# Kernel tuning notes

Measured on AMD Instinct MI355X. Metric: run time of the kernel, lower is better.

Reference implementation:

```python
import jax, jax.numpy as jnp
import numpy as np

N = 50000   # nodes per channel
E = 800000  # edges per channel
F = 128     # node feature dim
H = 4       # heads
C = 32      # per-head channels (output_dim // heads = 128 // 4)
D = H * C   # output_dim = 128
B = 64      # graphs in batch


def gatv2_conv(x, edge_index, Wl, bl, Wr, br, att, bias):
    """PyG GATv2Conv (share_weights=False, add_self_loops=True, neg_slope=0.2),
    eval mode (attention dropout disabled)."""
    n = x.shape[0]
    loops = jnp.arange(n, dtype=edge_index.dtype)
    src = jnp.concatenate([edge_index[0], loops])  # [E+N]
    dst = jnp.concatenate([edge_index[1], loops])
    xl = (x @ Wl + bl).reshape(n, H, C)  # source transform
    xr = (x @ Wr + br).reshape(n, H, C)  # target transform
    s = xl[src] + xr[dst]                              # [E+N, H, C]
    e = jnp.einsum('ehc,hc->eh', jax.nn.leaky_relu(s, 0.2), att)  # [E+N, H]
    emax = jax.ops.segment_max(e, dst, num_segments=n)            # softmax over incoming edges
    ee = jnp.exp(e - emax[dst])
    denom = jax.ops.segment_sum(ee, dst, num_segments=n)
    alpha = ee / jnp.maximum(denom[dst], 1e-16)                   # [E+N, H]
    out = jax.ops.segment_sum(alpha[:, :, None] * xl[src], dst, num_segments=n)  # [N, H, C]
    return out.reshape(n, D) + bias


def gep(x, batch, num_graphs):
    """global_mean_pool"""
    s = jax.ops.segment_sum(x, batch, num_segments=num_graphs)
    cnt = jax.ops.segment_sum(jnp.ones((x.shape[0],), x.dtype), batch, num_segments=num_graphs)
    return s / jnp.maximum(cnt, 1.0)[:, None]


def lrelu(x):  # nn.LeakyReLU() default slope 0.01
    return jax.nn.leaky_relu(x, 0.01)


def _branch_params(key, scale=0.05):
    ks = jax.random.split(key, 8)
    return dict(
        Wl=jax.random.normal(ks[0], (F, D), jnp.float32) * scale,
        bl=jnp.zeros((D,), jnp.float32),
        Wr=jax.random.normal(ks[1], (F, D), jnp.float32) * scale,
        br=jnp.zeros((D,), jnp.float32),
        att=jax.random.normal(ks[2], (H, C), jnp.float32) * scale,
        bias=jnp.zeros((D,), jnp.float32),
        fcW=jax.random.normal(ks[3], (D, D), jnp.float32) * scale,
        fcb=jnp.zeros((D,), jnp.float32),
    )


def setup_inputs() -> dict:
    key = jax.random.key(0)
    k = jax.random.split(key, 12)
    inp = {
        'ch1_x': jax.random.normal(k[0], (N, F), jnp.float32),
        'ch1_edge_index': jax.random.randint(k[1], (2, E), 0, N, jnp.int32),
        'ch1_batch': jnp.sort(jax.random.randint(k[2], (N,), 0, B, jnp.int32)),
        'ch2_x': jax.random.normal(k[3], (N, F), jnp.float32),
        'ch2_edge_index': jax.random.randint(k[4], (2, E), 0, N, jnp.int32),
        'ch2_batch': jnp.sort(jax.random.randint(k[5], (N,), 0, B, jnp.int32)),
    }
    p1 = _branch_params(k[6]); p2 = _branch_params(k[7])
    for name, v in p1.items():
        inp['p1_' + name] = v
    for name, v in p2.items():
        inp['p2_' + name] = v
    inp['fc1_W'] = jax.random.normal(k[8], (2 * D, D), jnp.float32) * 0.05
    inp['fc1_b'] = jnp.zeros((D,), jnp.float32)
    inp['fc2_W'] = jax.random.normal(k[9], (D, 16), jnp.float32) * 0.05
    inp['fc2_b'] = jnp.zeros((16,), jnp.float32)
    inp['out_W'] = jax.random.normal(k[10], (16, 1), jnp.float32) * 0.05
    inp['out_b'] = jnp.zeros((1,), jnp.float32)
    return inp


def reference(ch1_x, ch1_edge_index, ch1_batch, ch2_x, ch2_edge_index, ch2_batch,
              p1_Wl, p1_bl, p1_Wr, p1_br, p1_att, p1_bias, p1_fcW, p1_fcb,
              p2_Wl, p2_bl, p2_Wr, p2_br, p2_att, p2_bias, p2_fcW, p2_fcb,
              fc1_W, fc1_b, fc2_W, fc2_b, out_W, out_b):
    # branch 1 (dropout = identity in eval mode)
    x = gatv2_conv(ch1_x, ch1_edge_index, p1_Wl, p1_bl, p1_Wr, p1_br, p1_att, p1_bias)
    x = lrelu(x)
    x = gep(x, ch1_batch, B)
    x = lrelu(x @ p1_fcW + p1_fcb)
    # branch 2
    xt = gatv2_conv(ch2_x, ch2_edge_index, p2_Wl, p2_bl, p2_Wr, p2_br, p2_att, p2_bias)
    xt = lrelu(xt)
    xt = gep(xt, ch2_batch, B)
    xt = lrelu(xt @ p2_fcW + p2_fcb)
    # head
    xc = jnp.concatenate([x, xt], axis=1)          # [B, 2D]
    xc = lrelu(xc @ fc1_W + fc1_b)
    xc = lrelu(xc @ fc2_W + fc2_b)
    return xc @ out_W + out_b                      # [B, 1]
```

## Files before the change

### kernel.cpp

```cpp
#include <hip/hip_runtime.h>
#include <hip/hip_bf16.h>
#include <math.h>

#define F_DIM 128
#define B_GRAPHS 64
#define AGG_WAVES 8

__device__ __forceinline__ float lrelu(float v, float s) {
    return v > 0.f ? v : s * v;
}

__device__ __forceinline__ int lower_bound_i(const int* __restrict__ a, int n, int v) {
    int lo = 0, hi = n;
    while (lo < hi) {
        int mid = (lo + hi) >> 1;
        if (a[mid] < v) lo = mid + 1; else hi = mid;
    }
    return lo;
}

__global__ void count2_k(const int* __restrict__ ei0, const int* __restrict__ ei1,
                         int* __restrict__ c0, int* __restrict__ c1, int E) {
    const int* ei = blockIdx.y ? ei1 : ei0;
    int* cnt = blockIdx.y ? c1 : c0;
    int i = blockIdx.x * blockDim.x + threadIdx.x;
    if (i < E) atomicAdd(cnt + ei[E + i], 1);
}

__global__ __launch_bounds__(1024) void scan2_k(const int* __restrict__ c0,
                                                const int* __restrict__ c1,
                                                int* __restrict__ s0, int* __restrict__ s1,
                                                int n, int tot) {
    const int* cnt = blockIdx.x ? c1 : c0;
    int* start = blockIdx.x ? s1 : s0;
    __shared__ int ssum[1024];
    int t = threadIdx.x;
    int chunk = (n + 1023) / 1024;
    int lo = t * chunk, hi = min(lo + chunk, n);
    int s = 0;
    for (int i = lo; i < hi; ++i) s += cnt[i] + 1;
    ssum[t] = s;
    __syncthreads();
    for (int offs = 1; offs < 1024; offs <<= 1) {
        int v = (t >= offs) ? ssum[t - offs] : 0;
        __syncthreads();
        ssum[t] += v;
        __syncthreads();
    }
    int excl = (t == 0) ? 0 : ssum[t - 1];
    for (int i = lo; i < hi; ++i) {
        start[i] = excl;
        excl += cnt[i] + 1;
    }
    if (t == 1023) start[n] = tot;
}

__global__ __launch_bounds__(256) void gemm2_bias_scatter(
        const float* __restrict__ A,
        const float* __restrict__ Wl, const float* __restrict__ bl,
        const float* __restrict__ Wr, const float* __restrict__ br,
        float* __restrict__ Cl, float* __restrict__ Cr, int n,
        const int* __restrict__ ei0, const int* __restrict__ ei1,
        const int* __restrict__ st0, const int* __restrict__ st1,
        int* __restrict__ c0, int* __restrict__ c1,
        int* __restrict__ ss0, int* __restrict__ ss1,
        int E, int tot, int ipb) {
    int base = blockIdx.x * ipb;
    int lim = min(base + ipb, 2 * tot);
    int pos_0 = -1, pos_1 = -1, pos_2 = -1;
    int src_0 = 0, src_1 = 0, src_2 = 0;
    int* ssp_0 = ss0; int* ssp_1 = ss0; int* ssp_2 = ss0;
    #pragma unroll
    for (int q = 0; q < 3; ++q) {
        int it = base + q * 256 + (int)threadIdx.x;
        if (it < lim) {
            int ch = (it >= tot) ? 1 : 0;
            int local = it - (ch ? tot : 0);
            const int* ei = ch ? ei1 : ei0;
            const int* st = ch ? st1 : st0;
            int* cnt = ch ? c1 : c0;
            int* ss = ch ? ss1 : ss0;
            int pos, src;
            if (local < n) {
                pos = st[local];
                src = local;
            } else {
                int j = local - n;
                int dst = ei[E + j];
                src = ei[j];
                int o = atomicAdd(cnt + dst, -1);
                pos = st[dst] + o;
            }
            if (q == 0) { pos_0 = pos; src_0 = src; ssp_0 = ss; }
            if (q == 1) { pos_1 = pos; src_1 = src; ssp_1 = ss; }
            if (q == 2) { pos_2 = pos; src_2 = src; ssp_2 = ss; }
        }
    }
    for (int it = base + 768 + (int)threadIdx.x; it < lim; it += 256) {
        int ch = (it >= tot) ? 1 : 0;
        int local = it - (ch ? tot : 0);
        const int* ei = ch ? ei1 : ei0;
        const int* st = ch ? st1 : st0;
        int* cnt = ch ? c1 : c0;
        int* ss = ch ? ss1 : ss0;
        if (local < n) ss[st[local]] = local;
        else {
            int j = local - n;
            int dst = ei[E + j];
            int o = atomicAdd(cnt + dst, -1);
            ss[st[dst] + o] = ei[j];
        }
    }

    __shared__ float As[16][F_DIM];
    int row0 = blockIdx.x * 16;
    for (int i = threadIdx.x; i < 16 * F_DIM; i += 256) {
        int r = i >> 7, c = i & 127;
        int gr = row0 + r;
        As[r][c] = (gr < n) ? A[(size_t)gr * F_DIM + c] : 0.f;
    }
    __syncthreads();
    int c = threadIdx.x & 127;
    int rg = (threadIdx.x >> 7) * 8;
    float accl[8] = {0.f, 0.f, 0.f, 0.f, 0.f, 0.f, 0.f, 0.f};
    float accr[8] = {0.f, 0.f, 0.f, 0.f, 0.f, 0.f, 0.f, 0.f};
    for (int k = 0; k < F_DIM; k += 4) {
        float wl0 = Wl[(k + 0) * F_DIM + c];
        float wl1 = Wl[(k + 1) * F_DIM + c];
        float wl2 = Wl[(k + 2) * F_DIM + c];
        float wl3 = Wl[(k + 3) * F_DIM + c];
        float wr0 = Wr[(k + 0) * F_DIM + c];
        float wr1 = Wr[(k + 1) * F_DIM + c];
        float wr2 = Wr[(k + 2) * F_DIM + c];
        float wr3 = Wr[(k + 3) * F_DIM + c];
        #pragma unroll
        for (int j = 0; j < 8; ++j) {
            float4 a = *(const float4*)&As[rg + j][k];
            accl[j] += a.x * wl0 + a.y * wl1 + a.z * wl2 + a.w * wl3;
            accr[j] += a.x * wr0 + a.y * wr1 + a.z * wr2 + a.w * wr3;
        }
    }
    #pragma unroll
    for (int j = 0; j < 8; ++j) {
        int r = row0 + rg + j;
        if (r < n) {
            Cl[(size_t)r * F_DIM + c] = accl[j] + bl[c];
            Cr[(size_t)r * F_DIM + c] = accr[j] + br[c];
        }
    }

    if (pos_0 >= 0) ssp_0[pos_0] = src_0;
    if (pos_1 >= 0) ssp_1[pos_1] = src_1;
    if (pos_2 >= 0) ssp_2[pos_2] = src_2;
}

__global__ __launch_bounds__(256) void gemm2_bias(
        const float* __restrict__ A,
        const float* __restrict__ Wl, const float* __restrict__ bl,
        const float* __restrict__ Wr, const float* __restrict__ br,
        float* __restrict__ Cl, float* __restrict__ Cr, int n) {
    __shared__ float As[16][F_DIM];
    int row0 = blockIdx.x * 16;
    for (int i = threadIdx.x; i < 16 * F_DIM; i += 256) {
        int r = i >> 7, c = i & 127;
        int gr = row0 + r;
        As[r][c] = (gr < n) ? A[(size_t)gr * F_DIM + c] : 0.f;
    }
    __syncthreads();
    int c = threadIdx.x & 127;
    int rg = (threadIdx.x >> 7) * 8;
    float accl[8] = {0.f, 0.f, 0.f, 0.f, 0.f, 0.f, 0.f, 0.f};
    float accr[8] = {0.f, 0.f, 0.f, 0.f, 0.f, 0.f, 0.f, 0.f};
    for (int k = 0; k < F_DIM; k += 4) {
        float wl0 = Wl[(k + 0) * F_DIM + c];
        float wl1 = Wl[(k + 1) * F_DIM + c];
        float wl2 = Wl[(k + 2) * F_DIM + c];
        float wl3 = Wl[(k + 3) * F_DIM + c];
        float wr0 = Wr[(k + 0) * F_DIM + c];
        float wr1 = Wr[(k + 1) * F_DIM + c];
        float wr2 = Wr[(k + 2) * F_DIM + c];
        float wr3 = Wr[(k + 3) * F_DIM + c];
        #pragma unroll
        for (int j = 0; j < 8; ++j) {
            float4 a = *(const float4*)&As[rg + j][k];
            accl[j] += a.x * wl0 + a.y * wl1 + a.z * wl2 + a.w * wl3;
            accr[j] += a.x * wr0 + a.y * wr1 + a.z * wr2 + a.w * wr3;
        }
    }
    #pragma unroll
    for (int j = 0; j < 8; ++j) {
        int r = row0 + rg + j;
        if (r < n) {
            Cl[(size_t)r * F_DIM + c] = accl[j] + bl[c];
            Cr[(size_t)r * F_DIM + c] = accr[j] + br[c];
        }
    }
}

__global__ __launch_bounds__(512) void gat_agg(
        const float* __restrict__ xl, const float* __restrict__ xr,
        const float* __restrict__ att, const float* __restrict__ bias,
        const int* __restrict__ start, const int* __restrict__ sortedSrc,
        const int* __restrict__ batch, float* __restrict__ pool, int n) {
    __shared__ float accs[AGG_WAVES][F_DIM];
    __shared__ int gids[AGG_WAVES];
    int lane = threadIdx.x & 63;
    int w = threadIdx.x >> 6;
    int node = blockIdx.x * AGG_WAVES + w;

    float v0 = 0.f, v1 = 0.f;
    if (node < n) {
        float2 b   = *(const float2*)(xr + (size_t)node * F_DIM + 2 * lane);
        float  at0 = att[2 * lane];
        float  at1 = att[2 * lane + 1];
        int s = start[node];
        int e = start[node + 1];

        float d = 0.f, a0 = 0.f, a1 = 0.f;
        int i = s;
        for (; i + 4 <= e; i += 4) {
            int s0 = sortedSrc[i + 0];
            int s1 = sortedSrc[i + 1];
            int s2 = sortedSrc[i + 2];
            int s3 = sortedSrc[i + 3];
            float2 A0 = *(const float2*)(xl + (size_t)s0 * F_DIM + 2 * lane);
            float2 A1 = *(const float2*)(xl + (size_t)s1 * F_DIM + 2 * lane);
            float2 A2 = *(const float2*)(xl + (size_t)s2 * F_DIM + 2 * lane);
            float2 A3 = *(const float2*)(xl + (size_t)s3 * F_DIM + 2 * lane);
            float p0 = lrelu(A0.x + b.x, 0.2f) * at0 + lrelu(A0.y + b.y, 0.2f) * at1;
            float p1 = lrelu(A1.x + b.x, 0.2f) * at0 + lrelu(A1.y + b.y, 0.2f) * at1;
            float p2 = lrelu(A2.x + b.x, 0.2f) * at0 + lrelu(A2.y + b.y, 0.2f) * at1;
            float p3 = lrelu(A3.x + b.x, 0.2f) * at0 + lrelu(A3.y + b.y, 0.2f) * at1;
            #pragma unroll
            for (int sh = 1; sh <= 8; sh <<= 1) {
                p0 += __shfl_xor(p0, sh);
                p1 += __shfl_xor(p1, sh);
                p2 += __shfl_xor(p2, sh);
                p3 += __shfl_xor(p3, sh);
            }
            float w0 = __expf(p0);
            float w1 = __expf(p1);
            float w2 = __expf(p2);
            float w3 = __expf(p3);
            d  += (w0 + w1) + (w2 + w3);
            a0 += (w0 * A0.x + w1 * A1.x) + (w2 * A2.x + w3 * A3.x);
            a1 += (w0 * A0.y + w1 * A1.y) + (w2 * A2.y + w3 * A3.y);
        }
        for (; i < e; ++i) {
            int src = sortedSrc[i];
            float2 A = *(const float2*)(xl + (size_t)src * F_DIM + 2 * lane);
            float p = lrelu(A.x + b.x, 0.2f) * at0 + lrelu(A.y + b.y, 0.2f) * at1;
            #pragma unroll
            for (int sh = 1; sh <= 8; sh <<= 1) p += __shfl_xor(p, sh);
            float wt = __expf(p);
            d  += wt;
            a0 += wt * A.x;
            a1 += wt * A.y;
        }
        float inv = 1.f / d;
        v0 = lrelu(a0 * inv + bias[2 * lane + 0], 0.01f);
        v1 = lrelu(a1 * inv + bias[2 * lane + 1], 0.01f);
        if (lane == 0) gids[w] = batch[node];
    } else {
        if (lane == 0) gids[w] = -1;
    }
    accs[w][2 * lane + 0] = v0;
    accs[w][2 * lane + 1] = v1;
    __syncthreads();

    if (threadIdx.x < F_DIM) {
        int t = threadIdx.x;
        float sum = 0.f;
        int cg = -1;
        #pragma unroll
        for (int r = 0; r < AGG_WAVES; ++r) {
            int g = gids[r];
            if (g < 0) continue;
            if (g != cg) {
                if (cg >= 0) atomicAdd(pool + (size_t)cg * F_DIM + t, sum);
                sum = 0.f;
                cg = g;
            }
            sum += accs[r][t];
        }
        if (cg >= 0) atomicAdd(pool + (size_t)cg * F_DIM + t, sum);
    }
}

__global__ void branch_fc2(const float* __restrict__ pool0, const float* __restrict__ pool1,
                           const int* __restrict__ batch0, const int* __restrict__ batch1,
                           const float* __restrict__ W0, const float* __restrict__ b0,
                           const float* __restrict__ W1, const float* __restrict__ b1,
                           float* __restrict__ out0, float* __restrict__ out1, int n) {
    int ch = blockIdx.x >> 6;
    int g  = blockIdx.x & 63;
    const float* pool  = ch ? pool1 : pool0;
    const int*   batch = ch ? batch1 : batch0;
    const float* W     = ch ? W1 : W0;
    const float* b     = ch ? b1 : b0;
    float*       out   = ch ? out1 : out0;

    int lo = lower_bound_i(batch, n, g);
    int hi = lower_bound_i(batch, n, g + 1);
    float c = fmaxf((float)(hi - lo), 1.f);

    __shared__ float xm[F_DIM];
    int j = threadIdx.x;
    xm[j] = pool[(size_t)g * F_DIM + j] / c;
    __syncthreads();
    float acc = b[j];
    for (int k = 0; k < F_DIM; ++k) acc += xm[k] * W[k * F_DIM + j];
    out[(size_t)g * F_DIM + j] = lrelu(acc, 0.01f);
}

__global__ void head_k(const float* __restrict__ x1, const float* __restrict__ x2,
                       const float* __restrict__ W1, const float* __restrict__ b1,
                       const float* __restrict__ W2, const float* __restrict__ b2,
                       const float* __restrict__ Wo, const float* __restrict__ bo,
                       float* __restrict__ out) {
    int g = blockIdx.x;
    int t = threadIdx.x;
    __shared__ float xc[2 * F_DIM];
    __shared__ float h1[F_DIM];
    __shared__ float h2[16];
    xc[t] = (t < F_DIM) ? x1[(size_t)g * F_DIM + t] : x2[(size_t)g * F_DIM + (t - F_DIM)];
    __syncthreads();
    if (t < F_DIM) {
        float acc = b1[t];
        for (int k = 0; k < 2 * F_DIM; ++k) acc += xc[k] * W1[k * F_DIM + t];
        h1[t] = lrelu(acc, 0.01f);
    }
    __syncthreads();
    if (t < 16) {
        float acc = b2[t];
        for (int k = 0; k < F_DIM; ++k) acc += h1[k] * W2[k * 16 + t];
        h2[t] = lrelu(acc, 0.01f);
    }
    __syncthreads();
    if (t == 0) {
        float acc = bo[0];
        for (int k = 0; k < 16; ++k) acc += h2[k] * Wo[k];
        out[g] = acc;
    }
}

extern "C" void kernel_launch(void* const* d_in, const int* in_sizes, int n_in,
                              void* d_out, int out_size, void* d_ws, size_t ws_size,
                              hipStream_t stream) {
    const int N = in_sizes[0] / F_DIM;
    const int E = in_sizes[1] / 2;
    const int TOT = E + N;

    const int* ei0    = (const int*)d_in[1];
    const int* ei1    = (const int*)d_in[4];
    const int* batch0 = (const int*)d_in[2];
    const int* batch1 = (const int*)d_in[5];

    float* w = (float*)d_ws;
    size_t off = 0;
    float* xl   = w + off; off += (size_t)N * F_DIM;
    float* xr   = w + off; off += (size_t)N * F_DIM;
    float* xfc0 = w + off; off += (size_t)B_GRAPHS * F_DIM;
    float* xfc1 = w + off; off += (size_t)B_GRAPHS * F_DIM;
    int* ss0    = (int*)(w + off); off += (size_t)TOT;
    int* ss1    = (int*)(w + off); off += (size_t)TOT;
    int* st0    = (int*)(w + off); off += (size_t)(N + 1);
    int* st1    = (int*)(w + off); off += (size_t)(N + 1);
    float* pool0 = w + off;
    float* pool1 = pool0 + (size_t)B_GRAPHS * F_DIM;
    int*   cnt0  = (int*)(pool1 + (size_t)B_GRAPHS * F_DIM);
    int*   cnt1  = cnt0 + N;
    const size_t zeroBytes = (2 * (size_t)B_GRAPHS * F_DIM + 2 * (size_t)N) * 4;

    const int edgeBlocks = (E + 255) / 256;
    const int gemmBlocks = (N + 15) / 16;
    const int aggBlocks  = (N + AGG_WAVES - 1) / AGG_WAVES;
    const int ipb = (2 * TOT + gemmBlocks - 1) / gemmBlocks;

    hipMemsetAsync(pool0, 0, zeroBytes, stream);
    hipLaunchKernelGGL(count2_k, dim3(edgeBlocks, 2), dim3(256), 0, stream,
                       ei0, ei1, cnt0, cnt1, E);
    hipLaunchKernelGGL(scan2_k, dim3(2), dim3(1024), 0, stream,
                       cnt0, cnt1, st0, st1, N, TOT);

    hipLaunchKernelGGL(gemm2_bias_scatter, dim3(gemmBlocks), dim3(256), 0, stream,
                       (const float*)d_in[0],
                       (const float*)d_in[6], (const float*)d_in[7],
                       (const float*)d_in[8], (const float*)d_in[9],
                       xl, xr, N,
                       ei0, ei1, st0, st1, cnt0, cnt1, ss0, ss1, E, TOT, ipb);
    hipLaunchKernelGGL(gat_agg, dim3(aggBlocks), dim3(512), 0, stream,
                       xl, xr, (const float*)d_in[10], (const float*)d_in[11],
                       st0, ss0, batch0, pool0, N);

    hipLaunchKernelGGL(gemm2_bias, dim3(gemmBlocks), dim3(256), 0, stream,
                       (const float*)d_in[3],
                       (const float*)d_in[14], (const float*)d_in[15],
                       (const float*)d_in[16], (const float*)d_in[17],
                       xl, xr, N);
    hipLaunchKernelGGL(gat_agg, dim3(aggBlocks), dim3(512), 0, stream,
                       xl, xr, (const float*)d_in[18], (const float*)d_in[19],
                       st1, ss1, batch1, pool1, N);

    hipLaunchKernelGGL(branch_fc2, dim3(2 * B_GRAPHS), dim3(F_DIM), 0, stream,
                       pool0, pool1, batch0, batch1,
                       (const float*)d_in[12], (const float*)d_in[13],
                       (const float*)d_in[20], (const float*)d_in[21],
                       xfc0, xfc1, N);

    hipLaunchKernelGGL(head_k, dim3(B_GRAPHS), dim3(256), 0, stream,
                       xfc0, xfc1,
                       (const float*)d_in[22], (const float*)d_in[23],
                       (const float*)d_in[24], (const float*)d_in[25],
                       (const float*)d_in[26], (const float*)d_in[27],
                       (float*)d_out);
}
```

Measured before the change: 673.2 us.

## Process four destination nodes per wave with LDS accumulators and prefetched indices

The GAT aggregation kernel now handles 32 nodes per block, and each wave walks the concatenated edge range of four consecutive destination nodes instead of one. Per-node xr rows, weighted accumulators and softmax denominators are kept in shared memory, and source indices are prefetched one iteration ahead. The aim is to balance uneven per-node degrees within a wave, cut tail-loop waste and reduce per-block overhead. In exchange, shared-memory read-modify-writes are added in the inner loop, the lane-to-feature mapping changes from float2 loads to two scalar loads, and LDS use grows, which may lower occupancy.

```diff
diff --git a/kernel.cpp b/kernel.cpp
--- a/kernel.cpp
+++ b/kernel.cpp
@@ -4,7 +4,8 @@
 
 #define F_DIM 128
 #define B_GRAPHS 64
-#define AGG_WAVES 8
+#define AGG_NODES 32
+#define AGG_NPW 4
 
 __device__ __forceinline__ float lrelu(float v, float s) {
     return v > 0.f ? v : s * v;
@@ -197,93 +198,99 @@
     }
 }
 
-__global__ __launch_bounds__(512) void gat_agg(
+__global__ __launch_bounds__(512) void gat_agg_v9(
         const float* __restrict__ xl, const float* __restrict__ xr,
         const float* __restrict__ att, const float* __restrict__ bias,
-        const int* __restrict__ start, const int* __restrict__ sortedSrc,
+        const int* __restrict__ start, const int* __restrict__ ss,
         const int* __restrict__ batch, float* __restrict__ pool, int n) {
-    __shared__ float accs[AGG_WAVES][F_DIM];
-    __shared__ int gids[AGG_WAVES];
-    int lane = threadIdx.x & 63;
-    int w = threadIdx.x >> 6;
-    int node = blockIdx.x * AGG_WAVES + w;
-
-    float v0 = 0.f, v1 = 0.f;
-    if (node < n) {
-        float2 b   = *(const float2*)(xr + (size_t)node * F_DIM + 2 * lane);
-        float  at0 = att[2 * lane];
-        float  at1 = att[2 * lane + 1];
-        int s = start[node];
-        int e = start[node + 1];
-
-        float d = 0.f, a0 = 0.f, a1 = 0.f;
-        int i = s;
-        for (; i + 4 <= e; i += 4) {
-            int s0 = sortedSrc[i + 0];
-            int s1 = sortedSrc[i + 1];
-            int s2 = sortedSrc[i + 2];
-            int s3 = sortedSrc[i + 3];
-            float2 A0 = *(const float2*)(xl + (size_t)s0 * F_DIM + 2 * lane);
-            float2 A1 = *(const float2*)(xl + (size_t)s1 * F_DIM + 2 * lane);
-            float2 A2 = *(const float2*)(xl + (size_t)s2 * F_DIM + 2 * lane);
-            float2 A3 = *(const float2*)(xl + (size_t)s3 * F_DIM + 2 * lane);
-            float p0 = lrelu(A0.x + b.x, 0.2f) * at0 + lrelu(A0.y + b.y, 0.2f) * at1;
-            float p1 = lrelu(A1.x + b.x, 0.2f) * at0 + lrelu(A1.y + b.y, 0.2f) * at1;
-            float p2 = lrelu(A2.x + b.x, 0.2f) * at0 + lrelu(A2.y + b.y, 0.2f) * at1;
-            float p3 = lrelu(A3.x + b.x, 0.2f) * at0 + lrelu(A3.y + b.y, 0.2f) * at1;
+    __shared__ float xrs[F_DIM][AGG_NODES + 1];
+    __shared__ float acc[F_DIM][AGG_NODES + 1];
+    __shared__ float dvs[4][AGG_NODES + 8];
+    __shared__ int gb[AGG_NODES];
+
+    int base = blockIdx.x * AGG_NODES;
+    int nodes = min(AGG_NODES, n - base);
+    int tid = threadIdx.x;
+
+    for (int i = tid; i < F_DIM * (AGG_NODES + 1); i += 512) ((float*)acc)[i] = 0.f;
+    if (tid < 4 * (AGG_NODES + 8)) ((float*)dvs)[tid] = 0.f;
+    if (tid < nodes) gb[tid] = batch[base + tid];
+    {
+        int col = tid & 127, r0 = tid >> 7;
+        for (int row = r0; row < nodes; row += 4)
+            xrs[col][row] = xr[(size_t)(base + row) * F_DIM + col];
+    }
+    __syncthreads();
+
+    int wv = tid >> 6, l = tid & 63;
+    float at0 = att[l], at1 = att[64 + l];
+
+    int nb = wv * AGG_NPW;
+    int lim = min(AGG_NPW, nodes - nb);
+    if (lim > 0) {
+        int b0 = start[base + nb];
+        int b1 = start[base + nb + min(1, lim)];
+        int b2 = start[base + nb + min(2, lim)];
+        int b3 = start[base + nb + min(3, lim)];
+        int iend = start[base + nb + lim];
+
+        int nsrc[4];
+        #pragma unroll
+        for (int q = 0; q < 4; ++q) nsrc[q] = ss[min(b0 + q, iend - 1)];
+
+        for (int i = b0; i < iend; i += 4) {
+            int csrc[4];
             #pragma unroll
-            for (int sh = 1; sh <= 8; sh <<= 1) {
-                p0 += __shfl_xor(p0, sh);
-                p1 += __shfl_xor(p1, sh);
-                p2 += __shfl_xor(p2, sh);
-                p3 += __shfl_xor(p3, sh);
+            for (int q = 0; q < 4; ++q) csrc[q] = nsrc[q];
+            #pragma unroll
+            for (int q = 0; q < 4; ++q) nsrc[q] = ss[min(i + 4 + q, iend - 1)];
+            float g0[4], g1[4];
+            #pragma unroll
+            for (int q = 0; q < 4; ++q) {
+                const float* p = xl + (size_t)csrc[q] * F_DIM;
+                g0[q] = p[l];
+                g1[q] = p[64 + l];
             }
-            float w0 = __expf(p0);
-            float w1 = __expf(p1);
-            float w2 = __expf(p2);
-            float w3 = __expf(p3);
-            d  += (w0 + w1) + (w2 + w3);
-            a0 += (w0 * A0.x + w1 * A1.x) + (w2 * A2.x + w3 * A3.x);
-            a1 += (w0 * A0.y + w1 * A1.y) + (w2 * A2.y + w3 * A3.y);
-        }
-        for (; i < e; ++i) {
-            int src = sortedSrc[i];
-            float2 A = *(const float2*)(xl + (size_t)src * F_DIM + 2 * lane);
-            float p = lrelu(A.x + b.x, 0.2f) * at0 + lrelu(A.y + b.y, 0.2f) * at1;
             #pragma unroll
-            for (int sh = 1; sh <= 8; sh <<= 1) p += __shfl_xor(p, sh);
-            float wt = __expf(p);
-            d  += wt;
-            a0 += wt * A.x;
-            a1 += wt * A.y;
-        }
-        float inv = 1.f / d;
-        v0 = lrelu(a0 * inv + bias[2 * lane + 0], 0.01f);
-        v1 = lrelu(a1 * inv + bias[2 * lane + 1], 0.01f);
-        if (lane == 0) gids[w] = batch[node];
-    } else {
-        if (lane == 0) gids[w] = -1;
-    }
-    accs[w][2 * lane + 0] = v0;
-    accs[w][2 * lane + 1] = v1;
-    __syncthreads();
-
-    if (threadIdx.x < F_DIM) {
-        int t = threadIdx.x;
-        float sum = 0.f;
-        int cg = -1;
-        #pragma unroll
-        for (int r = 0; r < AGG_WAVES; ++r) {
-            int g = gids[r];
-            if (g < 0) continue;
+            for (int q = 0; q < 4; ++q) {
+                int it = i + q;
+                if (it >= iend) break;
+                int k = (it >= b1) + (it >= b2) + (it >= b3);
+                int dl = nb + k;
+                float pa = lrelu(g0[q] + xrs[l][dl], 0.2f) * at0;
+                float pb = lrelu(g1[q] + xrs[64 + l][dl], 0.2f) * at1;
+                pa += __shfl_xor(pa, 1);  pb += __shfl_xor(pb, 1);
+                pa += __shfl_xor(pa, 2);  pb += __shfl_xor(pb, 2);
+                pa += __shfl_xor(pa, 4);  pb += __shfl_xor(pb, 4);
+                pa += __shfl_xor(pa, 8);  pb += __shfl_xor(pb, 8);
+                pa += __shfl_xor(pa, 16); pb += __shfl_xor(pb, 16);
+                float wa = __expf(pa);
+                float wb = __expf(pb);
+                acc[l][dl]      += wa * g0[q];
+                acc[64 + l][dl] += wb * g1[q];
+                if ((l & 31) == 0) {
+                    dvs[l >> 5][dl]       += wa;
+                    dvs[2 + (l >> 5)][dl] += wb;
+                }
+            }
+        }
+    }
+    __syncthreads();
+
+    {
+        int c = tid & 127, part = tid >> 7;
+        int d0 = part * 8, d1 = min(d0 + 8, nodes);
+        float sum = 0.f; int cg = -1;
+        for (int dl = d0; dl < d1; ++dl) {
+            float v = lrelu(acc[c][dl] / dvs[c >> 5][dl] + bias[c], 0.01f);
+            int g = gb[dl];
             if (g != cg) {
-                if (cg >= 0) atomicAdd(pool + (size_t)cg * F_DIM + t, sum);
-                sum = 0.f;
-                cg = g;
+                if (cg >= 0) atomicAdd(pool + (size_t)cg * F_DIM + c, sum);
+                sum = 0.f; cg = g;
             }
-            sum += accs[r][t];
-        }
-        if (cg >= 0) atomicAdd(pool + (size_t)cg * F_DIM + t, sum);
+            sum += v;
+        }
+        if (cg >= 0) atomicAdd(pool + (size_t)cg * F_DIM + c, sum);
     }
 }
 
@@ -374,7 +381,7 @@
 
     const int edgeBlocks = (E + 255) / 256;
     const int gemmBlocks = (N + 15) / 16;
-    const int aggBlocks  = (N + AGG_WAVES - 1) / AGG_WAVES;
+    const int aggBlocks  = (N + AGG_NODES - 1) / AGG_NODES;
     const int ipb = (2 * TOT + gemmBlocks - 1) / gemmBlocks;
 
     hipMemsetAsync(pool0, 0, zeroBytes, stream);
@@ -389,7 +396,7 @@
                        (const float*)d_in[8], (const float*)d_in[9],
                        xl, xr, N,
                        ei0, ei1, st0, st1, cnt0, cnt1, ss0, ss1, E, TOT, ipb);
-    hipLaunchKernelGGL(gat_agg, dim3(aggBlocks), dim3(512), 0, stream,
+    hipLaunchKernelGGL(gat_agg_v9, dim3(aggBlocks), dim3(512), 0, stream,
                        xl, xr, (const float*)d_in[10], (const float*)d_in[11],
                        st0, ss0, batch0, pool0, N);
 
@@ -398,7 +405,7 @@
                        (const float*)d_in[14], (const float*)d_in[15],
                        (const float*)d_in[16], (const float*)d_in[17],
                        xl, xr, N);
-    hipLaunchKernelGGL(gat_agg, dim3(aggBlocks), dim3(512), 0, stream,
+    hipLaunchKernelGGL(gat_agg_v9, dim3(aggBlocks), dim3(512), 0, stream,
                        xl, xr, (const float*)d_in[18], (const float*)d_in[19],
                        st1, ss1, batch1, pool1, N);
 
```

Result: slower. 829.4 us (+23.2%).
